# Performance work log

Hardware: AMD Instinct MI355X
Metric: run time of the kernel (lower is better)

The kernel has to match this reference:

```python
import jax, jax.numpy as jnp
import numpy as np

BATCH, IN, HID, OMID, OUT = 8192, 64, 1024, 128, 1
MAX_ITER = 8
EPS = 1e-3


def setup_inputs() -> dict:
    key = jax.random.key(0)
    ks = jax.random.split(key, 32)
    s_in, s_h = 1.0 / np.sqrt(IN), 1.0 / np.sqrt(HID)
    d = {"x": jax.random.normal(ks[0], (BATCH, IN), jnp.float32)}
    names = ["i", "f", "c", "o"]
    for j, n in enumerate(names):
        d[f"Wx{n}"] = jax.random.uniform(ks[1 + 4 * j], (HID, IN), jnp.float32, -s_in, s_in)
        d[f"bx{n}"] = jax.random.uniform(ks[2 + 4 * j], (HID,), jnp.float32, -s_in, s_in)
        d[f"Wh{n}"] = jax.random.uniform(ks[3 + 4 * j], (HID, HID), jnp.float32, -s_h, s_h)
        d[f"bh{n}"] = jax.random.uniform(ks[4 + 4 * j], (HID,), jnp.float32, -s_h, s_h)
    d["W_halt"] = jax.random.uniform(ks[20], (1, HID), jnp.float32, -s_h, s_h)
    d["b_halt"] = jax.random.uniform(ks[21], (1,), jnp.float32, -s_h, s_h)
    d["W1"] = jax.random.uniform(ks[22], (OMID, HID), jnp.float32, -s_h, s_h)
    d["b1"] = jax.random.uniform(ks[23], (OMID,), jnp.float32, -s_h, s_h)
    s_m = 1.0 / np.sqrt(OMID)
    d["W2"] = jax.random.uniform(ks[24], (OUT, OMID), jnp.float32, -s_m, s_m)
    d["b2"] = jax.random.uniform(ks[25], (OUT,), jnp.float32, -s_m, s_m)
    return d


def _act_forward(x, Wxi, bxi, Whi, bhi, Wxf, bxf, Whf, bhf, Wxc, bxc, Whc, bhc,
                 Wxo, bxo, Who, bho, W_halt, b_halt, W1, b1, W2, b2):
    B = x.shape[0]
    state0 = jnp.zeros((B, HID), x.dtype)
    cell0 = jnp.zeros((B, HID), x.dtype)
    p0 = jnp.zeros((B,), x.dtype)
    active0 = jnp.ones((B,), bool)

    def step(carry, t):
        state, cell, p_sum, active = carry
        # four LSTM-style gates (computed dense; masked update == torch's gather/scatter)
        i_g = jax.nn.sigmoid(x @ Wxi.T + bxi + state @ Whi.T + bhi)
        f_g = jax.nn.sigmoid(x @ Wxf.T + bxf + state @ Whf.T + bhf)
        c_g = jnp.tanh(x @ Wxc.T + bxc + state @ Whc.T + bhc)
        o_g = jax.nn.sigmoid(x @ Wxo.T + bxo + state @ Who.T + bho)
        am = active[:, None]
        cell = jnp.where(am, f_g * cell + i_g * c_g, cell)
        state = jnp.where(am, o_g * jnp.tanh(cell), state)
        out = jax.nn.sigmoid(jax.nn.relu(state @ W1.T + b1) @ W2.T + b2)  # (B, OUT)
        h = jax.nn.sigmoid(state @ W_halt.T + b_halt)[:, 0]               # (B,)
        p_new = p_sum + h
        last = t == MAX_ITER - 1
        finished = active & ((p_new >= 1.0 - EPS) | last)
        halt_rec = jnp.where(finished, 1.0 - p_sum, jnp.where(active, h, 0.0))
        p_sum = jnp.where(finished, 1.0, jnp.where(active, p_new, p_sum))
        out_rec = jnp.where(am, out, 0.0)
        active = active & ~finished
        return (state, cell, p_sum, active), (out_rec, halt_rec)

    _, (outs, halts) = jax.lax.scan(step, (state0, cell0, p0, active0), jnp.arange(MAX_ITER))
    # outs: (T, B, OUT), halts: (T, B); final = sum_t out_t * p_halt_t
    return jnp.einsum("tbo,tb->bo", outs, halts)


def reference(x, Wxi, bxi, Whi, bhi, Wxf, bxf, Whf, bhf, Wxc, bxc, Whc, bhc,
              Wxo, bxo, Who, bho, W_halt, b_halt, W1, b1, W2, b2):
    return _act_forward(x, Wxi, bxi, Whi, bhi, Wxf, bxf, Whf, bhf, Wxc, bxc, Whc, bhc,
                        Wxo, bxo, Who, bho, W_halt, b_halt, W1, b1, W2, b2)
```

## Files before the change

### kernel.cpp

```cpp
#include <hip/hip_runtime.h>
#include <hip/hip_bf16.h>

#define BATCH 8192
#define IN_DIM 64
#define HID 1024
#define KTOT 1088
#define NGATES 4096
#define OMID 128
#define NP 256
#define MAX_ITER 8

#define TM 128
#define TN 128
#define TK 64
#define GTM 256
#define GTN 256
#define TAILB 64

typedef __attribute__((ext_vector_type(8))) short short8;
typedef __attribute__((ext_vector_type(4))) float float4v;

__device__ __forceinline__ float bf2f(short s) {
    union { float f; unsigned u; } v; v.u = ((unsigned)(unsigned short)s) << 16; return v.f;
}
__device__ __forceinline__ short f2bf(float f) {
    union { float f; unsigned u; } v; v.f = f;
    unsigned r = v.u + 0x7fff + ((v.u >> 16) & 1);
    return (short)(r >> 16);
}
__device__ __forceinline__ float sigmoidf_(float x) {
    float xc = fminf(fmaxf(x, -30.f), 30.f);
    return 1.f / (1.f + __expf(-xc));
}
__device__ __forceinline__ float tanhf_(float x) {
    float xc = fminf(fmaxf(x, -15.f), 15.f);
    float e = __expf(2.f * xc);
    return (e - 1.f) / (e + 1.f);
}
__device__ __forceinline__ int aload(const int* p) {
    return __hip_atomic_load((int*)p, __ATOMIC_RELAXED, __HIP_MEMORY_SCOPE_AGENT);
}
__device__ __forceinline__ void astore(int* p, int v) {
    __hip_atomic_store(p, v, __ATOMIC_RELAXED, __HIP_MEMORY_SCOPE_AGENT);
}

__device__ __forceinline__ void gbar(int* bar, int phase, int tid) {
    __syncthreads();
    if (tid == 0) {
        __threadfence();
        __hip_atomic_fetch_add(bar, 1, __ATOMIC_ACQ_REL, __HIP_MEMORY_SCOPE_AGENT);
        while (aload(bar) < TAILB * phase)
            __builtin_amdgcn_s_sleep(8);
        __threadfence();
    }
    __syncthreads();
}

__device__ __forceinline__ void gates_epilogue(
    const float4v (&acc)[4][4], int m0, int bx, int wave, int lane, int first,
    const float* __restrict__ bias_g, float* __restrict__ cell,
    short* __restrict__ Sout, const int* __restrict__ ridx, int n_act)
{
    const int wm = wave & 1, wn = wave >> 1;
    const int colq = lane & 15, q = lane >> 4;
    const int G = bx * 2 + wn;
    const int h = G * 16 + colq;
    const float bi  = bias_g[G * 64 +  0 + colq];
    const float bff = bias_g[G * 64 + 16 + colq];
    const float bc  = bias_g[G * 64 + 32 + colq];
    const float bo  = bias_g[G * 64 + 48 + colq];
#pragma unroll
    for (int i = 0; i < 4; ++i) {
        const int pbase = m0 + wm * 64 + i * 16 + q * 4;
#pragma unroll
        for (int r = 0; r < 4; ++r) {
            const int pos = pbase + r;
            if (pos < n_act) {
                const int row = ridx[pos];
                const float ig = sigmoidf_(acc[i][0][r] + bi);
                const float fg = sigmoidf_(acc[i][1][r] + bff);
                const float cg = tanhf_(acc[i][2][r] + bc);
                const float og = sigmoidf_(acc[i][3][r] + bo);
                const size_t ci = (size_t)row * HID + h;
                const float c = first ? (ig * cg) : (fg * cell[ci] + ig * cg);
                cell[ci] = c;
                Sout[(size_t)row * HID + h] = f2bf(og * tanhf_(c));
            }
        }
    }
}

__global__ __launch_bounds__(512, 1) void gates_k(
    const short* __restrict__ S, const short* __restrict__ XB,
    const short* __restrict__ B,
    const float* __restrict__ bias_g, int nK, int hidK, int first,
    float* __restrict__ cell, short* __restrict__ Sout,
    const int* __restrict__ ridx, const int* __restrict__ cnt, int t)
{
    __shared__ short As[2][GTM * TK];
    __shared__ short Bs[2][GTN * TK];
    const int n_act = cnt[t];
    const int tid  = threadIdx.x;
    const int wave = tid >> 6, lane = tid & 63;
    const int wm2 = wave >> 2, wn4 = wave & 3;
    const int colq = lane & 15, q = lane >> 4;
    const int lrow8 = lane >> 3;
    const int lk    = (((lane & 7) ^ lrow8) * 8);
    const int xq = colq & 7;
    const int abase = (wm2 * 128 + colq) * TK;
    const int bbase = (wn4 * 64  + colq) * TK;

    int bx, byS;
    {
        const int lin  = (int)blockIdx.x + 16 * (int)blockIdx.y;
        const int xcd  = lin & 7;
        const int slot = lin >> 3;
        bx  = (xcd & 1) * 8 + (slot & 7);
        byS = (xcd >> 1) * 4 + (slot >> 3);
    }
    const int n0 = bx * GTN;

    for (int by = byS; by * GTM < n_act; by += 16) {
        const int m0 = by * GTM;

        int arow[2][2];
        const short* bptr[2][2];
#pragma unroll
        for (int h = 0; h < 2; ++h)
#pragma unroll
            for (int l = 0; l < 2; ++l) {
                const int rr = h * 128 + wave * 16 + l * 8 + lrow8;
                arow[h][l] = ridx[m0 + rr];
                bptr[h][l] = B + (size_t)(n0 + rr) * KTOT + lk;
            }

        float4v acc[8][4];
#pragma unroll
        for (int i = 0; i < 8; ++i)
#pragma unroll
            for (int j = 0; j < 4; ++j) acc[i][j] = (float4v)0.f;

        auto stageA = [&](int kt, int h) {
            const int kk = kt * TK;
            const bool fromS = (kk < hidK);
#pragma unroll
            for (int l = 0; l < 2; ++l) {
                const int dst = (h * 128 + wave * 16 + l * 8) * TK;
                const short* sa = fromS
                    ? (S  + (size_t)arow[h][l] * HID    + kk + lk)
                    : (XB + (size_t)arow[h][l] * IN_DIM + lk);
                __builtin_amdgcn_global_load_lds(
                    (const __attribute__((address_space(1))) void*)sa,
                    (__attribute__((address_space(3))) void*)(As[kt & 1] + dst), 16, 0, 0);
            }
        };
        auto stageB = [&](int kt, int h) {
            const int kk = kt * TK;
#pragma unroll
            for (int l = 0; l < 2; ++l) {
                const int dst = (h * 128 + wave * 16 + l * 8) * TK;
                __builtin_amdgcn_global_load_lds(
                    (const __attribute__((address_space(1))) void*)(bptr[h][l] + kk),
                    (__attribute__((address_space(3))) void*)(Bs[kt & 1] + dst), 16, 0, 0);
            }
        };

        stageA(0, 0); stageA(0, 1); stageB(0, 0); stageB(0, 1);
        if (nK > 1) {
            stageA(1, 0); stageA(1, 1);
            asm volatile("s_waitcnt vmcnt(4)" ::: "memory");
        } else {
            asm volatile("s_waitcnt vmcnt(0)" ::: "memory");
        }
        asm volatile("s_barrier" ::: "memory");

        for (int kt = 0; kt < nK; ++kt) {
            const short* Ac = As[kt & 1];
            const short* Bc = Bs[kt & 1];
            const int xt0 = (q ^ xq) << 3;
            const int xt1 = ((q + 4) ^ xq) << 3;
            short8 af[8], bf[4];

#pragma unroll
            for (int i = 0; i < 8; ++i)
                af[i] = *(const short8*)(Ac + abase + i * (16 * TK) + xt0);
            bf[0] = *(const short8*)(Bc + bbase + 0 * (16 * TK) + xt0);
            bf[1] = *(const short8*)(Bc + bbase + 1 * (16 * TK) + xt0);
            if (kt + 1 < nK) stageB(kt + 1, 0);
            asm volatile("s_barrier" ::: "memory");
            asm volatile("s_waitcnt lgkmcnt(0)" ::: "memory");
            __builtin_amdgcn_sched_barrier(0);
            __builtin_amdgcn_s_setprio(1);
#pragma unroll
            for (int i = 0; i < 8; ++i) {
                acc[i][0] = __builtin_amdgcn_mfma_f32_16x16x32_bf16(af[i], bf[0], acc[i][0], 0, 0, 0);
                acc[i][1] = __builtin_amdgcn_mfma_f32_16x16x32_bf16(af[i], bf[1], acc[i][1], 0, 0, 0);
            }
            __builtin_amdgcn_s_setprio(0);
            asm volatile("s_barrier" ::: "memory");

            bf[2] = *(const short8*)(Bc + bbase + 2 * (16 * TK) + xt0);
            bf[3] = *(const short8*)(Bc + bbase + 3 * (16 * TK) + xt0);
            if (kt + 1 < nK) stageB(kt + 1, 1);
            asm volatile("s_barrier" ::: "memory");
            asm volatile("s_waitcnt lgkmcnt(0)" ::: "memory");
            __builtin_amdgcn_sched_barrier(0);
            __builtin_amdgcn_s_setprio(1);
#pragma unroll
            for (int i = 0; i < 8; ++i) {
                acc[i][2] = __builtin_amdgcn_mfma_f32_16x16x32_bf16(af[i], bf[2], acc[i][2], 0, 0, 0);
                acc[i][3] = __builtin_amdgcn_mfma_f32_16x16x32_bf16(af[i], bf[3], acc[i][3], 0, 0, 0);
            }
            __builtin_amdgcn_s_setprio(0);
            asm volatile("s_barrier" ::: "memory");

#pragma unroll
            for (int i = 0; i < 8; ++i)
                af[i] = *(const short8*)(Ac + abase + i * (16 * TK) + xt1);
            bf[0] = *(const short8*)(Bc + bbase + 0 * (16 * TK) + xt1);
            bf[1] = *(const short8*)(Bc + bbase + 1 * (16 * TK) + xt1);
            asm volatile("s_barrier" ::: "memory");
            asm volatile("s_waitcnt lgkmcnt(0)" ::: "memory");
            __builtin_amdgcn_sched_barrier(0);
            __builtin_amdgcn_s_setprio(1);
#pragma unroll
            for (int i = 0; i < 8; ++i) {
                acc[i][0] = __builtin_amdgcn_mfma_f32_16x16x32_bf16(af[i], bf[0], acc[i][0], 0, 0, 0);
                acc[i][1] = __builtin_amdgcn_mfma_f32_16x16x32_bf16(af[i], bf[1], acc[i][1], 0, 0, 0);
            }
            __builtin_amdgcn_s_setprio(0);
            asm volatile("s_barrier" ::: "memory");

            bf[2] = *(const short8*)(Bc + bbase + 2 * (16 * TK) + xt1);
            bf[3] = *(const short8*)(Bc + bbase + 3 * (16 * TK) + xt1);
            if (kt + 2 < nK) { stageA(kt + 2, 0); stageA(kt + 2, 1); }
            asm volatile("s_barrier" ::: "memory");
            asm volatile("s_waitcnt lgkmcnt(0)" ::: "memory");
            __builtin_amdgcn_sched_barrier(0);
            __builtin_amdgcn_s_setprio(1);
#pragma unroll
            for (int i = 0; i < 8; ++i) {
                acc[i][2] = __builtin_amdgcn_mfma_f32_16x16x32_bf16(af[i], bf[2], acc[i][2], 0, 0, 0);
                acc[i][3] = __builtin_amdgcn_mfma_f32_16x16x32_bf16(af[i], bf[3], acc[i][3], 0, 0, 0);
            }
            __builtin_amdgcn_s_setprio(0);
            if (kt + 2 < nK)
                asm volatile("s_waitcnt vmcnt(4)" ::: "memory");
            else
                asm volatile("s_waitcnt vmcnt(0)" ::: "memory");
            asm volatile("s_barrier" ::: "memory");
        }

        const int G = bx * 4 + wn4;
        const int h = G * 16 + colq;
        const float bi  = bias_g[G * 64 +  0 + colq];
        const float bff = bias_g[G * 64 + 16 + colq];
        const float bc  = bias_g[G * 64 + 32 + colq];
        const float bo  = bias_g[G * 64 + 48 + colq];
#pragma unroll
        for (int i = 0; i < 8; ++i) {
            const int pbase = m0 + wm2 * 128 + i * 16 + q * 4;
#pragma unroll
            for (int r = 0; r < 4; ++r) {
                const int pos = pbase + r;
                if (pos < n_act) {
                    const int row = ridx[pos];
                    const float ig = sigmoidf_(acc[i][0][r] + bi);
                    const float fg = sigmoidf_(acc[i][1][r] + bff);
                    const float cg = tanhf_(acc[i][2][r] + bc);
                    const float og = sigmoidf_(acc[i][3][r] + bo);
                    const size_t ci = (size_t)row * HID + h;
                    const float c = first ? (ig * cg) : (fg * cell[ci] + ig * cg);
                    cell[ci] = c;
                    Sout[(size_t)row * HID + h] = f2bf(og * tanhf_(c));
                }
            }
        }
    }
}

__device__ __forceinline__ void gates_tile(
    short* As, short* Bs, int tid,
    const short* __restrict__ S, const short* __restrict__ XB,
    const short* __restrict__ B,
    const float* __restrict__ bias_g,
    float* __restrict__ cell, short* __restrict__ Sout,
    const int* __restrict__ ridx, int n_act, int m0, int bx)
{
    const int wave = tid >> 6, lane = tid & 63;
    const int wm = wave & 1, wn = wave >> 1;
    const int colq = lane & 15, q = lane >> 4;
    const int lrow8 = lane >> 3;
    const int lk    = (((lane & 7) ^ lrow8) * 8);
    const int n0 = bx * TN;

    int aoff[4][2], boff[4][2];
#pragma unroll
    for (int i = 0; i < 4; ++i) {
        const int Ra = wm * 64 + i * 16 + colq;
        const int Rb = wn * 64 + i * 16 + colq;
#pragma unroll
        for (int c2 = 0; c2 < 2; ++c2) {
            const int C = q + 4 * c2;
            aoff[i][c2] = Ra * TK + ((C ^ (Ra & 7)) << 3);
            boff[i][c2] = Rb * TK + ((C ^ (Rb & 7)) << 3);
        }
    }

    float4v acc[4][4];
#pragma unroll
    for (int i = 0; i < 4; ++i)
#pragma unroll
        for (int j = 0; j < 4; ++j) acc[i][j] = (float4v)0.f;

    const short* gaS[4];
    const short* gaX[4];
    const short* gb[4];
#pragma unroll
    for (int it = 0; it < 4; ++it) {
        const int rr = (wave * 4 + it) * 8;
        const int r0 = ridx[m0 + rr + lrow8];
        gaS[it] = S + (size_t)r0 * HID + lk;
        gaX[it] = XB + (size_t)r0 * IN_DIM + lk;
        gb[it]  = B + (size_t)(n0 + rr + lrow8) * KTOT + lk;
    }

    for (int ki = 0; ki < KTOT / TK; ++ki) {
        const bool fromS = (ki * TK < HID);
#pragma unroll
        for (int it = 0; it < 4; ++it) {
            const int rr = (wave * 4 + it) * 8;
            const short* a0 = fromS ? gaS[it] : gaX[it];
            __builtin_amdgcn_global_load_lds(
                (const __attribute__((address_space(1))) void*)a0,
                (__attribute__((address_space(3))) void*)(As + rr * TK), 16, 0, 0);
            __builtin_amdgcn_global_load_lds(
                (const __attribute__((address_space(1))) void*)gb[it],
                (__attribute__((address_space(3))) void*)(Bs + rr * TK), 16, 0, 0);
            gaS[it] += TK; gb[it] += TK;
        }
        __syncthreads();
#pragma unroll
        for (int c2 = 0; c2 < 2; ++c2) {
            short8 af[4], bf[4];
#pragma unroll
            for (int i = 0; i < 4; ++i) {
                af[i] = *(const short8*)(As + aoff[i][c2]);
                bf[i] = *(const short8*)(Bs + boff[i][c2]);
            }
#pragma unroll
            for (int i = 0; i < 4; ++i)
#pragma unroll
                for (int j = 0; j < 4; ++j)
                    acc[i][j] = __builtin_amdgcn_mfma_f32_16x16x32_bf16(af[i], bf[j], acc[i][j], 0, 0, 0);
        }
        __syncthreads();
    }

    gates_epilogue(acc, m0, bx, wave, lane, 0, bias_g, cell, Sout, ridx, n_act);
    __syncthreads();
}

__device__ __forceinline__ void midfin_tile(
    short* As, short* Bs, int tid,
    const short* __restrict__ Snew, const short* __restrict__ P,
    const float* __restrict__ bias_p, const float* __restrict__ W_halt,
    const float* __restrict__ W2, const float* __restrict__ b2,
    float* __restrict__ outp, float* __restrict__ p_sum,
    const int* __restrict__ rprev, int* __restrict__ rnext,
    int* __restrict__ cnt, int t, int m0, int n_act)
{
    const int wave = tid >> 6, lane = tid & 63;
    const int wm = wave & 1, wn = wave >> 1;
    const int colq = lane & 15, q = lane >> 4;
    const int lrow8 = lane >> 3;
    const int lk    = (((lane & 7) ^ lrow8) * 8);

    float4v acc[4][4];
#pragma unroll
    for (int i = 0; i < 4; ++i)
#pragma unroll
        for (int j = 0; j < 4; ++j) acc[i][j] = (float4v)0.f;

    const short* ga[4];
    const short* gb[4];
#pragma unroll
    for (int it = 0; it < 4; ++it) {
        const int rr = (wave * 4 + it) * 8;
        ga[it] = Snew + (size_t)rprev[m0 + rr + lrow8] * HID + lk;
        gb[it] = P + (size_t)(rr + lrow8) * HID + lk;
    }
    int aoff[4][2], boff[4][2];
#pragma unroll
    for (int i = 0; i < 4; ++i) {
        const int Ra = wm * 64 + i * 16 + colq;
        const int Rb = wn * 64 + i * 16 + colq;
#pragma unroll
        for (int c2 = 0; c2 < 2; ++c2) {
            const int C = q + 4 * c2;
            aoff[i][c2] = Ra * TK + ((C ^ (Ra & 7)) << 3);
            boff[i][c2] = Rb * TK + ((C ^ (Rb & 7)) << 3);
        }
    }

    for (int k0 = 0; k0 < HID; k0 += TK) {
#pragma unroll
        for (int it = 0; it < 4; ++it) {
            const int rr = (wave * 4 + it) * 8;
            __builtin_amdgcn_global_load_lds(
                (const __attribute__((address_space(1))) void*)ga[it],
                (__attribute__((address_space(3))) void*)(As + rr * TK), 16, 0, 0);
            __builtin_amdgcn_global_load_lds(
                (const __attribute__((address_space(1))) void*)gb[it],
                (__attribute__((address_space(3))) void*)(Bs + rr * TK), 16, 0, 0);
            ga[it] += TK; gb[it] += TK;
        }
        __syncthreads();
#pragma unroll
        for (int c2 = 0; c2 < 2; ++c2) {
            short8 af[4], bf[4];
#pragma unroll
            for (int i = 0; i < 4; ++i) {
                af[i] = *(const short8*)(As + aoff[i][c2]);
                bf[i] = *(const short8*)(Bs + boff[i][c2]);
            }
#pragma unroll
            for (int i = 0; i < 4; ++i)
#pragma unroll
                for (int j = 0; j < 4; ++j)
                    acc[i][j] = __builtin_amdgcn_mfma_f32_16x16x32_bf16(af[i], bf[j], acc[i][j], 0, 0, 0);
        }
        __syncthreads();
    }

    float* red  = (float*)As;
    float* hbuf = ((float*)As) + 256;

    for (int s = 0; s < 32; ++s) {
        const int lr = wave * 32 + s;
        const int row = rprev[m0 + lr];
        const short* Ar = Snew + (size_t)row * HID + lane * 16;
        const short8 v0 = *(const short8*)Ar;
        const short8 v1 = *(const short8*)(Ar + 8);
        const float* Wh = W_halt + lane * 16;
        float hv = 0.f;
#pragma unroll
        for (int e = 0; e < 8; ++e) hv += bf2f(v0[e]) * Wh[e];
#pragma unroll
        for (int e = 0; e < 8; ++e) hv += bf2f(v1[e]) * Wh[8 + e];
#pragma unroll
        for (int o = 32; o > 0; o >>= 1) hv += __shfl_down(hv, o);
        if (lane == 0) hbuf[lr] = hv;
    }

    float pr[4][4];
#pragma unroll
    for (int i = 0; i < 4; ++i)
#pragma unroll
        for (int r = 0; r < 4; ++r) pr[i][r] = 0.f;
#pragma unroll
    for (int j = 0; j < 4; ++j) {
        const int col = wn * 64 + j * 16 + colq;
        const float b = bias_p[col];
        const float w2 = W2[col];
#pragma unroll
        for (int i = 0; i < 4; ++i)
#pragma unroll
            for (int r = 0; r < 4; ++r)
                pr[i][r] += fmaxf(acc[i][j][r] + b, 0.f) * w2;
    }
#pragma unroll
    for (int i = 0; i < 4; ++i)
#pragma unroll
        for (int r = 0; r < 4; ++r) {
            float v = pr[i][r];
            v += __shfl_down(v, 8, 16);
            v += __shfl_down(v, 4, 16);
            v += __shfl_down(v, 2, 16);
            v += __shfl_down(v, 1, 16);
            if (colq == 0)
                red[((((wn * 2) + wm) * 4 + i) * 4 + q) * 4 + r] = v;
        }
    __syncthreads();

    if (tid < TM) {
        const int pos = m0 + tid;
        if (pos < n_act) {
            const int lwm = tid >> 6, i = (tid >> 4) & 3, lq = (tid >> 2) & 3, r = tid & 3;
            const float odot = red[((lwm * 4 + i) * 4 + lq) * 4 + r]
                             + red[(((2 + lwm) * 4 + i) * 4 + lq) * 4 + r];
            const int row = rprev[pos];
            const float ov = sigmoidf_(odot + b2[0]);
            const float h  = sigmoidf_(hbuf[tid] + bias_p[OMID]);
            const float ps = p_sum[row];
            const float pn = ps + h;
            const bool fin = (pn >= 1.f - 1e-3f) || (t == MAX_ITER - 1);
            const float halt = fin ? (1.f - ps) : h;
            outp[row] += ov * halt;
            p_sum[row] = fin ? 1.f : pn;
            if (!fin) {
                const int d = atomicAdd(&cnt[t + 1], 1);
                astore(&rnext[d], row);
            }
        }
    }
    __syncthreads();
}

__global__ __launch_bounds__(256) void midfin_k(
    const short* __restrict__ Snew, const short* __restrict__ P,
    const float* __restrict__ bias_p, const float* __restrict__ W_halt,
    const float* __restrict__ W2, const float* __restrict__ b2,
    float* __restrict__ outp, float* __restrict__ p_sum,
    const int* __restrict__ rprev, int* __restrict__ rnext,
    int* __restrict__ cnt, int t)
{
    __shared__ short As[TM * TK];
    __shared__ short Bs[TN * TK];
    const int n_act = cnt[t];
    for (int tile = blockIdx.x; tile * TM < n_act; tile += gridDim.x)
        midfin_tile(As, Bs, threadIdx.x, Snew, P, bias_p, W_halt, W2, b2,
                    outp, p_sum, rprev, rnext, cnt, t, tile * TM, n_act);
}

__global__ __launch_bounds__(256) void tail_k(
    const short* __restrict__ Wg, const float* __restrict__ bias_g,
    const short* __restrict__ P, const float* __restrict__ bias_p,
    const float* __restrict__ W_halt, const float* __restrict__ W2,
    const float* __restrict__ b2,
    short* __restrict__ S0, short* __restrict__ S1,
    const short* __restrict__ XB,
    float* __restrict__ cell, float* __restrict__ outp,
    float* __restrict__ p_sum,
    int* __restrict__ ridx0, int* __restrict__ ridx1,
    int* __restrict__ cnt, int* __restrict__ bar)
{
    __shared__ short As[TM * TK];
    __shared__ short Bs[TN * TK];
    const int tid = threadIdx.x;
    int phase = 0;
    int t = 2;
    while (true) {
        short* Snew = (t & 1) ? S0 : S1;
        const int* rprev = (t & 1) ? ridx1 : ridx0;
        int* rnext = (t & 1) ? ridx0 : ridx1;
        const int n = aload(&cnt[t]);
        for (int tile = blockIdx.x; tile * TM < n; tile += gridDim.x)
            midfin_tile(As, Bs, tid, Snew, P, bias_p, W_halt, W2, b2,
                        outp, p_sum, rprev, rnext, cnt, t, tile * TM, n);
        if (t == MAX_ITER - 1) break;
        ++phase; gbar(bar, phase, tid);
        const int n1 = aload(&cnt[t + 1]);
        if (n1 == 0) break;
        {
            short* Sot = (t & 1) ? S1 : S0;
            const int ntiles = ((n1 + TM - 1) / TM) * (NGATES / TN);
            for (int e = blockIdx.x; e < ntiles; e += gridDim.x)
                gates_tile(As, Bs, tid, Snew, XB, Wg, bias_g, cell, Sot,
                           rnext, n1, (e >> 5) * TM, e & 31);
        }
        ++phase; gbar(bar, phase, tid);
        ++t;
    }
}

#define SETUP_XB    (BATCH * IN_DIM)
#define SETUP_WG    (NGATES * KTOT)
#define SETUP_P     (NP * HID)
#define SETUP_TOT   (SETUP_XB + SETUP_WG + SETUP_P)
__global__ __launch_bounds__(256) void setup_k(
    const float* __restrict__ x,
    const float* __restrict__ Whi, const float* __restrict__ Whf,
    const float* __restrict__ Whc, const float* __restrict__ Who,
    const float* __restrict__ Wxi, const float* __restrict__ Wxf,
    const float* __restrict__ Wxc, const float* __restrict__ Wxo,
    const float* __restrict__ bxi, const float* __restrict__ bhi,
    const float* __restrict__ bxf, const float* __restrict__ bhf,
    const float* __restrict__ bxc, const float* __restrict__ bhc,
    const float* __restrict__ bxo, const float* __restrict__ bho,
    const float* __restrict__ W1, const float* __restrict__ b1,
    const float* __restrict__ W_halt, const float* __restrict__ b_halt,
    short* __restrict__ XB,
    float* __restrict__ p_sum,
    int* __restrict__ ridx0, int* __restrict__ ridx1, int* __restrict__ cnt,
    int* __restrict__ bar, float* __restrict__ outp,
    short* __restrict__ Wg, float* __restrict__ bias_g,
    short* __restrict__ P, float* __restrict__ bias_p)
{
    int idx = blockIdx.x * 256 + threadIdx.x;
    if (idx < SETUP_XB) {
        const int row = idx >> 6, k = idx & 63;
        XB[idx] = f2bf(x[idx]);
        if (k == 0) {
            p_sum[row] = 0.f;
            outp[row] = 0.f;
            ridx0[row] = row;
            ridx1[row] = 0;
        }
        if (row == 0 && k <= MAX_ITER) cnt[k] = (k == 0) ? BATCH : 0;
        if (row == 1 && k == 0) bar[0] = 0;
        return;
    }
    idx -= SETUP_XB;
    if (idx < SETUP_WG) {
        const int n = idx / KTOT, k = idx - n * KTOT;
        const int G = n >> 6, g = (n >> 4) & 3, q = n & 15;
        const int h = G * 16 + q;
        const float* Wh = (g == 0) ? Whi : (g == 1) ? Whf : (g == 2) ? Whc : Who;
        const float* Wx = (g == 0) ? Wxi : (g == 1) ? Wxf : (g == 2) ? Wxc : Wxo;
        const float v = (k < HID) ? Wh[h * HID + k] : Wx[h * IN_DIM + (k - HID)];
        Wg[idx] = f2bf(v);
        if (k == 0) {
            const float* bx = (g == 0) ? bxi : (g == 1) ? bxf : (g == 2) ? bxc : bxo;
            const float* bh = (g == 0) ? bhi : (g == 1) ? bhf : (g == 2) ? bhc : bho;
            bias_g[n] = bx[h] + bh[h];
        }
        return;
    }
    idx -= SETUP_WG;
    if (idx < SETUP_P) {
        const int n = idx >> 10, k = idx & 1023;
        const float v = (n < OMID) ? W1[n * HID + k] : (n == OMID ? W_halt[k] : 0.f);
        P[idx] = f2bf(v);
        if (k == 0) bias_p[n] = (n < OMID) ? b1[n] : (n == OMID ? b_halt[0] : 0.f);
    }
}

extern "C" void kernel_launch(void* const* d_in, const int* in_sizes, int n_in,
                              void* d_out, int out_size, void* d_ws, size_t ws_size,
                              hipStream_t stream) {
    const float* x    = (const float*)d_in[0];
    const float* Wxi  = (const float*)d_in[1];
    const float* bxi  = (const float*)d_in[2];
    const float* Whi  = (const float*)d_in[3];
    const float* bhi  = (const float*)d_in[4];
    const float* Wxf  = (const float*)d_in[5];
    const float* bxf  = (const float*)d_in[6];
    const float* Whf  = (const float*)d_in[7];
    const float* bhf  = (const float*)d_in[8];
    const float* Wxc  = (const float*)d_in[9];
    const float* bxc  = (const float*)d_in[10];
    const float* Whc  = (const float*)d_in[11];
    const float* bhc  = (const float*)d_in[12];
    const float* Wxo  = (const float*)d_in[13];
    const float* bxo  = (const float*)d_in[14];
    const float* Who  = (const float*)d_in[15];
    const float* bho  = (const float*)d_in[16];
    const float* W_halt = (const float*)d_in[17];
    const float* b_halt = (const float*)d_in[18];
    const float* W1   = (const float*)d_in[19];
    const float* b1   = (const float*)d_in[20];
    const float* W2   = (const float*)d_in[21];
    const float* b2   = (const float*)d_in[22];

    char* p = (char*)d_ws;
    auto carve = [&](size_t bytes) { char* r = p; p += (bytes + 255) & ~(size_t)255; return r; };
    short* S0     = (short*)carve((size_t)BATCH * HID * 2);
    short* S1     = (short*)carve((size_t)BATCH * HID * 2);
    short* XB     = (short*)carve((size_t)BATCH * IN_DIM * 2);
    short* Wg     = (short*)carve((size_t)NGATES * KTOT * 2);
    float* bias_g = (float*)carve((size_t)NGATES * 4);
    short* P      = (short*)carve((size_t)NP * HID * 2);
    float* bias_p = (float*)carve((size_t)NP * 4);
    float* cell   = (float*)carve((size_t)BATCH * HID * 4);
    float* p_sum  = (float*)carve((size_t)BATCH * 4);
    int*   ridx0  = (int*)carve((size_t)BATCH * 4);
    int*   ridx1  = (int*)carve((size_t)BATCH * 4);
    int*   cnt    = (int*)carve((size_t)(MAX_ITER + 1) * 4);
    int*   bar    = (int*)carve(256);
    float* outp   = (float*)d_out;

    setup_k<<<(SETUP_TOT + 255) / 256, 256, 0, stream>>>(
        x, Whi, Whf, Whc, Who, Wxi, Wxf, Wxc, Wxo,
        bxi, bhi, bxf, bhf, bxc, bhc, bxo, bho,
        W1, b1, W_halt, b_halt,
        XB, p_sum, ridx0, ridx1, cnt, bar, outp,
        Wg, bias_g, P, bias_p);

    gates_k<<<dim3(16, 16), 512, 0, stream>>>(
        S0, XB, Wg + HID, bias_g, 1, 0, 1, cell, S1, ridx0, cnt, 0);
    midfin_k<<<64, 256, 0, stream>>>(
        S1, P, bias_p, W_halt, W2, b2, outp, p_sum, ridx0, ridx1, cnt, 0);
    gates_k<<<dim3(16, 16), 512, 0, stream>>>(
        S1, XB, Wg, bias_g, KTOT / TK, HID, 0, cell, S0, ridx1, cnt, 1);
    midfin_k<<<64, 256, 0, stream>>>(
        S0, P, bias_p, W_halt, W2, b2, outp, p_sum, ridx1, ridx0, cnt, 1);
    gates_k<<<dim3(16, 16), 512, 0, stream>>>(
        S0, XB, Wg, bias_g, KTOT / TK, HID, 0, cell, S1, ridx0, cnt, 2);
    tail_k<<<TAILB, 256, 0, stream>>>(
        Wg, bias_g, P, bias_p, W_halt, W2, b2,
        S0, S1, XB, cell, outp, p_sum, ridx0, ridx1, cnt, bar);
}
```

Before: 474.5 us.

## Shrink midfin row tile to 32, widen its grid, vectorise setup conversion

The mid/final projection tile drops from 128 to 32 batch rows. Each wave now covers a 32-column slice of the 128 W1 columns, with a four-way cross-wave reduction, and midfin_k launches 256 blocks instead of 64, so more CUs share the work. The setup kernel converts weights and inputs to bf16 four elements at a time with vector loads and stores. Scheduling barriers are added after each MFMA group in the gates GEMM. Smaller tiles reload the full P matrix more often per row, which raises P traffic, and the tail kernel's midfin loop also uses the smaller tiles.

```diff
diff --git a/kernel.cpp b/kernel.cpp
--- a/kernel.cpp
+++ b/kernel.cpp
@@ -13,12 +13,15 @@
 #define TM 128
 #define TN 128
 #define TK 64
+#define TMF 32
 #define GTM 256
 #define GTN 256
 #define TAILB 64
 
 typedef __attribute__((ext_vector_type(8))) short short8;
 typedef __attribute__((ext_vector_type(4))) float float4v;
+typedef __attribute__((ext_vector_type(4))) float float4f;
+typedef __attribute__((ext_vector_type(4))) short short4v;
 
 __device__ __forceinline__ float bf2f(short s) {
     union { float f; unsigned u; } v; v.u = ((unsigned)(unsigned short)s) << 16; return v.f;
@@ -197,6 +200,7 @@
                 acc[i][1] = __builtin_amdgcn_mfma_f32_16x16x32_bf16(af[i], bf[1], acc[i][1], 0, 0, 0);
             }
             __builtin_amdgcn_s_setprio(0);
+            __builtin_amdgcn_sched_barrier(0);
             asm volatile("s_barrier" ::: "memory");
 
             bf[2] = *(const short8*)(Bc + bbase + 2 * (16 * TK) + xt0);
@@ -212,6 +216,7 @@
                 acc[i][3] = __builtin_amdgcn_mfma_f32_16x16x32_bf16(af[i], bf[3], acc[i][3], 0, 0, 0);
             }
             __builtin_amdgcn_s_setprio(0);
+            __builtin_amdgcn_sched_barrier(0);
             asm volatile("s_barrier" ::: "memory");
 
 #pragma unroll
@@ -229,6 +234,7 @@
                 acc[i][1] = __builtin_amdgcn_mfma_f32_16x16x32_bf16(af[i], bf[1], acc[i][1], 0, 0, 0);
             }
             __builtin_amdgcn_s_setprio(0);
+            __builtin_amdgcn_sched_barrier(0);
             asm volatile("s_barrier" ::: "memory");
 
             bf[2] = *(const short8*)(Bc + bbase + 2 * (16 * TK) + xt1);
@@ -244,6 +250,7 @@
                 acc[i][3] = __builtin_amdgcn_mfma_f32_16x16x32_bf16(af[i], bf[3], acc[i][3], 0, 0, 0);
             }
             __builtin_amdgcn_s_setprio(0);
+            __builtin_amdgcn_sched_barrier(0);
             if (kt + 2 < nK)
                 asm volatile("s_waitcnt vmcnt(4)" ::: "memory");
             else
@@ -371,73 +378,58 @@
     int* __restrict__ cnt, int t, int m0, int n_act)
 {
     const int wave = tid >> 6, lane = tid & 63;
-    const int wm = wave & 1, wn = wave >> 1;
     const int colq = lane & 15, q = lane >> 4;
     const int lrow8 = lane >> 3;
     const int lk    = (((lane & 7) ^ lrow8) * 8);
-
-    float4v acc[4][4];
-#pragma unroll
-    for (int i = 0; i < 4; ++i)
-#pragma unroll
-        for (int j = 0; j < 4; ++j) acc[i][j] = (float4v)0.f;
-
-    const short* ga[4];
-    const short* gb[4];
-#pragma unroll
-    for (int it = 0; it < 4; ++it) {
-        const int rr = (wave * 4 + it) * 8;
-        ga[it] = Snew + (size_t)rprev[m0 + rr + lrow8] * HID + lk;
-        gb[it] = P + (size_t)(rr + lrow8) * HID + lk;
-    }
-    int aoff[4][2], boff[4][2];
-#pragma unroll
-    for (int i = 0; i < 4; ++i) {
-        const int Ra = wm * 64 + i * 16 + colq;
-        const int Rb = wn * 64 + i * 16 + colq;
+    const int xq = colq & 7;
+
+    float4v acc[2][2];
+#pragma unroll
+    for (int mi = 0; mi < 2; ++mi)
+#pragma unroll
+        for (int nj = 0; nj < 2; ++nj) acc[mi][nj] = (float4v)0.f;
+
+    const short* ga = Snew + (size_t)rprev[m0 + wave * 8 + lrow8] * HID + lk;
+    const short* gbp[4];
+#pragma unroll
+    for (int g = 0; g < 4; ++g)
+        gbp[g] = P + (size_t)(wave * 32 + g * 8 + lrow8) * HID + lk;
+
+    for (int k0 = 0; k0 < HID; k0 += TK) {
+        __builtin_amdgcn_global_load_lds(
+            (const __attribute__((address_space(1))) void*)(ga + k0),
+            (__attribute__((address_space(3))) void*)(As + (wave * 8) * TK), 16, 0, 0);
+#pragma unroll
+        for (int g = 0; g < 4; ++g)
+            __builtin_amdgcn_global_load_lds(
+                (const __attribute__((address_space(1))) void*)(gbp[g] + k0),
+                (__attribute__((address_space(3))) void*)(Bs + (wave * 32 + g * 8) * TK), 16, 0, 0);
+        __syncthreads();
 #pragma unroll
         for (int c2 = 0; c2 < 2; ++c2) {
-            const int C = q + 4 * c2;
-            aoff[i][c2] = Ra * TK + ((C ^ (Ra & 7)) << 3);
-            boff[i][c2] = Rb * TK + ((C ^ (Rb & 7)) << 3);
-        }
-    }
-
-    for (int k0 = 0; k0 < HID; k0 += TK) {
-#pragma unroll
-        for (int it = 0; it < 4; ++it) {
-            const int rr = (wave * 4 + it) * 8;
-            __builtin_amdgcn_global_load_lds(
-                (const __attribute__((address_space(1))) void*)ga[it],
-                (__attribute__((address_space(3))) void*)(As + rr * TK), 16, 0, 0);
-            __builtin_amdgcn_global_load_lds(
-                (const __attribute__((address_space(1))) void*)gb[it],
-                (__attribute__((address_space(3))) void*)(Bs + rr * TK), 16, 0, 0);
-            ga[it] += TK; gb[it] += TK;
+            const int xt = ((q + 4 * c2) ^ xq) << 3;
+            short8 af[2], bf[2];
+#pragma unroll
+            for (int mi = 0; mi < 2; ++mi)
+                af[mi] = *(const short8*)(As + (mi * 16 + colq) * TK + xt);
+#pragma unroll
+            for (int nj = 0; nj < 2; ++nj)
+                bf[nj] = *(const short8*)(Bs + (wave * 32 + nj * 16 + colq) * TK + xt);
+#pragma unroll
+            for (int mi = 0; mi < 2; ++mi)
+#pragma unroll
+                for (int nj = 0; nj < 2; ++nj)
+                    acc[mi][nj] = __builtin_amdgcn_mfma_f32_16x16x32_bf16(af[mi], bf[nj], acc[mi][nj], 0, 0, 0);
         }
         __syncthreads();
-#pragma unroll
-        for (int c2 = 0; c2 < 2; ++c2) {
-            short8 af[4], bf[4];
-#pragma unroll
-            for (int i = 0; i < 4; ++i) {
-                af[i] = *(const short8*)(As + aoff[i][c2]);
-                bf[i] = *(const short8*)(Bs + boff[i][c2]);
-            }
-#pragma unroll
-            for (int i = 0; i < 4; ++i)
-#pragma unroll
-                for (int j = 0; j < 4; ++j)
-                    acc[i][j] = __builtin_amdgcn_mfma_f32_16x16x32_bf16(af[i], bf[j], acc[i][j], 0, 0, 0);
-        }
-        __syncthreads();
     }
 
     float* red  = (float*)As;
-    float* hbuf = ((float*)As) + 256;
-
-    for (int s = 0; s < 32; ++s) {
-        const int lr = wave * 32 + s;
+    float* hbuf = ((float*)As) + 128;
+
+#pragma unroll
+    for (int s = 0; s < 8; ++s) {
+        const int lr = wave * 8 + s;
         const int row = rprev[m0 + lr];
         const short* Ar = Snew + (size_t)row * HID + lane * 16;
         const short8 v0 = *(const short8*)Ar;
@@ -453,42 +445,44 @@
         if (lane == 0) hbuf[lr] = hv;
     }
 
-    float pr[4][4];
-#pragma unroll
-    for (int i = 0; i < 4; ++i)
-#pragma unroll
-        for (int r = 0; r < 4; ++r) pr[i][r] = 0.f;
-#pragma unroll
-    for (int j = 0; j < 4; ++j) {
-        const int col = wn * 64 + j * 16 + colq;
+    float pr[2][4];
+#pragma unroll
+    for (int mi = 0; mi < 2; ++mi)
+#pragma unroll
+        for (int r = 0; r < 4; ++r) pr[mi][r] = 0.f;
+#pragma unroll
+    for (int nj = 0; nj < 2; ++nj) {
+        const int col = wave * 32 + nj * 16 + colq;
         const float b = bias_p[col];
         const float w2 = W2[col];
 #pragma unroll
-        for (int i = 0; i < 4; ++i)
+        for (int mi = 0; mi < 2; ++mi)
 #pragma unroll
             for (int r = 0; r < 4; ++r)
-                pr[i][r] += fmaxf(acc[i][j][r] + b, 0.f) * w2;
-    }
-#pragma unroll
-    for (int i = 0; i < 4; ++i)
+                pr[mi][r] += fmaxf(acc[mi][nj][r] + b, 0.f) * w2;
+    }
+#pragma unroll
+    for (int mi = 0; mi < 2; ++mi)
 #pragma unroll
         for (int r = 0; r < 4; ++r) {
-            float v = pr[i][r];
+            float v = pr[mi][r];
             v += __shfl_down(v, 8, 16);
             v += __shfl_down(v, 4, 16);
             v += __shfl_down(v, 2, 16);
             v += __shfl_down(v, 1, 16);
             if (colq == 0)
-                red[((((wn * 2) + wm) * 4 + i) * 4 + q) * 4 + r] = v;
+                red[((wave * 2 + mi) * 4 + q) * 4 + r] = v;
         }
     __syncthreads();
 
-    if (tid < TM) {
+    if (tid < TMF) {
         const int pos = m0 + tid;
         if (pos < n_act) {
-            const int lwm = tid >> 6, i = (tid >> 4) & 3, lq = (tid >> 2) & 3, r = tid & 3;
-            const float odot = red[((lwm * 4 + i) * 4 + lq) * 4 + r]
-                             + red[(((2 + lwm) * 4 + i) * 4 + lq) * 4 + r];
+            const int mi = tid >> 4, lq = (tid >> 2) & 3, r = tid & 3;
+            float odot = 0.f;
+#pragma unroll
+            for (int w = 0; w < 4; ++w)
+                odot += red[((w * 2 + mi) * 4 + lq) * 4 + r];
             const int row = rprev[pos];
             const float ov = sigmoidf_(odot + b2[0]);
             const float h  = sigmoidf_(hbuf[tid] + bias_p[OMID]);
@@ -518,9 +512,9 @@
     __shared__ short As[TM * TK];
     __shared__ short Bs[TN * TK];
     const int n_act = cnt[t];
-    for (int tile = blockIdx.x; tile * TM < n_act; tile += gridDim.x)
+    for (int tile = blockIdx.x; tile * TMF < n_act; tile += gridDim.x)
         midfin_tile(As, Bs, threadIdx.x, Snew, P, bias_p, W_halt, W2, b2,
-                    outp, p_sum, rprev, rnext, cnt, t, tile * TM, n_act);
+                    outp, p_sum, rprev, rnext, cnt, t, tile * TMF, n_act);
 }
 
 __global__ __launch_bounds__(256) void tail_k(
@@ -545,9 +539,9 @@
         const int* rprev = (t & 1) ? ridx1 : ridx0;
         int* rnext = (t & 1) ? ridx0 : ridx1;
         const int n = aload(&cnt[t]);
-        for (int tile = blockIdx.x; tile * TM < n; tile += gridDim.x)
+        for (int tile = blockIdx.x; tile * TMF < n; tile += gridDim.x)
             midfin_tile(As, Bs, tid, Snew, P, bias_p, W_halt, W2, b2,
-                        outp, p_sum, rprev, rnext, cnt, t, tile * TM, n);
+                        outp, p_sum, rprev, rnext, cnt, t, tile * TMF, n);
         if (t == MAX_ITER - 1) break;
         ++phase; gbar(bar, phase, tid);
         const int n1 = aload(&cnt[t + 1]);
@@ -564,10 +558,10 @@
     }
 }
 
-#define SETUP_XB    (BATCH * IN_DIM)
-#define SETUP_WG    (NGATES * KTOT)
-#define SETUP_P     (NP * HID)
-#define SETUP_TOT   (SETUP_XB + SETUP_WG + SETUP_P)
+#define SETUP_XB4   (BATCH * IN_DIM / 4)
+#define SETUP_WG4   (NGATES * (KTOT / 4))
+#define SETUP_P4    (NP * (HID / 4))
+#define SETUP_TOT4  (SETUP_XB4 + SETUP_WG4 + SETUP_P4)
 __global__ __launch_bounds__(256) void setup_k(
     const float* __restrict__ x,
     const float* __restrict__ Whi, const float* __restrict__ Whf,
@@ -588,41 +582,58 @@
     short* __restrict__ P, float* __restrict__ bias_p)
 {
     int idx = blockIdx.x * 256 + threadIdx.x;
-    if (idx < SETUP_XB) {
-        const int row = idx >> 6, k = idx & 63;
-        XB[idx] = f2bf(x[idx]);
-        if (k == 0) {
+    if (idx < SETUP_XB4) {
+        const int row = idx >> 4, k4 = (idx & 15) * 4;
+        const float4f v = *(const float4f*)(x + row * IN_DIM + k4);
+        short4v o;
+#pragma unroll
+        for (int e = 0; e < 4; ++e) o[e] = f2bf(v[e]);
+        *(short4v*)(XB + row * IN_DIM + k4) = o;
+        if (k4 == 0) {
             p_sum[row] = 0.f;
             outp[row] = 0.f;
             ridx0[row] = row;
             ridx1[row] = 0;
         }
-        if (row == 0 && k <= MAX_ITER) cnt[k] = (k == 0) ? BATCH : 0;
-        if (row == 1 && k == 0) bar[0] = 0;
+        if (idx == 0) {
+            for (int k = 0; k <= MAX_ITER; ++k) cnt[k] = (k == 0) ? BATCH : 0;
+            bar[0] = 0;
+        }
         return;
     }
-    idx -= SETUP_XB;
-    if (idx < SETUP_WG) {
-        const int n = idx / KTOT, k = idx - n * KTOT;
-        const int G = n >> 6, g = (n >> 4) & 3, q = n & 15;
-        const int h = G * 16 + q;
+    idx -= SETUP_XB4;
+    if (idx < SETUP_WG4) {
+        const int n = idx / (KTOT / 4), k4 = (idx - n * (KTOT / 4)) * 4;
+        const int G = n >> 6, g = (n >> 4) & 3, qq = n & 15;
+        const int h = G * 16 + qq;
         const float* Wh = (g == 0) ? Whi : (g == 1) ? Whf : (g == 2) ? Whc : Who;
         const float* Wx = (g == 0) ? Wxi : (g == 1) ? Wxf : (g == 2) ? Wxc : Wxo;
-        const float v = (k < HID) ? Wh[h * HID + k] : Wx[h * IN_DIM + (k - HID)];
-        Wg[idx] = f2bf(v);
-        if (k == 0) {
+        const float4f v = (k4 < HID)
+            ? *(const float4f*)(Wh + h * HID + k4)
+            : *(const float4f*)(Wx + h * IN_DIM + (k4 - HID));
+        short4v o;
+#pragma unroll
+        for (int e = 0; e < 4; ++e) o[e] = f2bf(v[e]);
+        *(short4v*)(Wg + (size_t)n * KTOT + k4) = o;
+        if (k4 == 0) {
             const float* bx = (g == 0) ? bxi : (g == 1) ? bxf : (g == 2) ? bxc : bxo;
             const float* bh = (g == 0) ? bhi : (g == 1) ? bhf : (g == 2) ? bhc : bho;
             bias_g[n] = bx[h] + bh[h];
         }
         return;
     }
-    idx -= SETUP_WG;
-    if (idx < SETUP_P) {
-        const int n = idx >> 10, k = idx & 1023;
-        const float v = (n < OMID) ? W1[n * HID + k] : (n == OMID ? W_halt[k] : 0.f);
-        P[idx] = f2bf(v);
-        if (k == 0) bias_p[n] = (n < OMID) ? b1[n] : (n == OMID ? b_halt[0] : 0.f);
+    idx -= SETUP_WG4;
+    if (idx < SETUP_P4) {
+        const int n = idx >> 8, k4 = (idx & 255) * 4;
+        float4f v;
+        if (n < OMID)      v = *(const float4f*)(W1 + n * HID + k4);
+        else if (n == OMID) v = *(const float4f*)(W_halt + k4);
+        else { v[0] = 0.f; v[1] = 0.f; v[2] = 0.f; v[3] = 0.f; }
+        short4v o;
+#pragma unroll
+        for (int e = 0; e < 4; ++e) o[e] = f2bf(v[e]);
+        *(short4v*)(P + (size_t)n * HID + k4) = o;
+        if (k4 == 0) bias_p[n] = (n < OMID) ? b1[n] : (n == OMID ? b_halt[0] : 0.f);
     }
 }
 
@@ -670,7 +681,7 @@
     int*   bar    = (int*)carve(256);
     float* outp   = (float*)d_out;
 
-    setup_k<<<(SETUP_TOT + 255) / 256, 256, 0, stream>>>(
+    setup_k<<<(SETUP_TOT4 + 255) / 256, 256, 0, stream>>>(
         x, Whi, Whf, Whc, Who, Wxi, Wxf, Wxc, Wxo,
         bxi, bhi, bxf, bhf, bxc, bhc, bxo, bho,
         W1, b1, W_halt, b_halt,
@@ -679,11 +690,11 @@
 
     gates_k<<<dim3(16, 16), 512, 0, stream>>>(
         S0, XB, Wg + HID, bias_g, 1, 0, 1, cell, S1, ridx0, cnt, 0);
-    midfin_k<<<64, 256, 0, stream>>>(
+    midfin_k<<<256, 256, 0, stream>>>(
         S1, P, bias_p, W_halt, W2, b2, outp, p_sum, ridx0, ridx1, cnt, 0);
     gates_k<<<dim3(16, 16), 512, 0, stream>>>(
         S1, XB, Wg, bias_g, KTOT / TK, HID, 0, cell, S0, ridx1, cnt, 1);
-    midfin_k<<<64, 256, 0, stream>>>(
+    midfin_k<<<256, 256, 0, stream>>>(
         S0, P, bias_p, W_halt, W2, b2, outp, p_sum, ridx1, ridx0, cnt, 1);
     gates_k<<<dim3(16, 16), 512, 0, stream>>>(
         S0, XB, Wg, bias_g, KTOT / TK, HID, 0, cell, S1, ridx0, cnt, 2);
```

Measured after the change: 450.9 us. -5.0%, faster.
